# Kernel optimization log

Hardware: AMD Instinct MI355X
Metric: run time of the kernel (lower is better)

## Reference

```python
import jax, jax.numpy as jnp
import numpy as np

EPS_NORM = 1e-12  # F.normalize eps

def _weight_norm(v, g):
    # torch weight_norm with dim=0: W[o,:] = g[o] * v[o,:] / ||v[o,:]||
    return g[:, None] * v / jnp.linalg.norm(v, axis=1, keepdims=True)

def _l2_normalize(x, axis):
    n = jnp.linalg.norm(x, axis=axis, keepdims=True)
    return x / jnp.maximum(n, EPS_NORM)

def setup_inputs() -> dict:
    key = jax.random.key(0)
    ks = jax.random.split(key, 6)
    B, C_emb, T = 16, 1024, 2048
    K, C_cb = 4096, 64
    return {
        "x": jax.random.normal(ks[0], (B, C_emb, T), dtype=jnp.float32),
        "v_in": jax.random.normal(ks[1], (C_cb, C_emb), dtype=jnp.float32) * 0.02,
        "g_in": jax.random.uniform(ks[2], (C_cb,), dtype=jnp.float32, minval=0.5, maxval=1.5),
        "v_out": jax.random.normal(ks[3], (C_emb, C_cb), dtype=jnp.float32) * 0.02,
        "g_out": jax.random.uniform(ks[4], (C_emb,), dtype=jnp.float32, minval=0.5, maxval=1.5),
        "codebook": jax.random.normal(ks[5], (K, C_cb), dtype=jnp.float32),
    }

def reference(x, v_in, g_in, v_out, g_out, codebook):
    sg = jax.lax.stop_gradient
    W_in = _weight_norm(v_in, g_in)    # (C_cb, C_emb)
    W_out = _weight_norm(v_out, g_out)  # (C_emb, C_cb)

    # 1x1 conv projection: (B, C_cb, T)
    x_proj = jnp.einsum('oi,bit->bot', W_in, x)

    # normalize=True: cosine-style nearest neighbor
    emb = _l2_normalize(x_proj, axis=1)           # (B, C_cb, T)
    cb_n = _l2_normalize(codebook, axis=1)        # (K, C_cb)

    e = jnp.swapaxes(emb, 1, 2)                   # (B, T, C_cb)
    # squared euclidean distance (monotone with cdist for argmin)
    dot = jnp.einsum('btc,kc->btk', e, cb_n)      # (B, T, K)
    d2 = (jnp.sum(e * e, axis=-1, keepdims=True)
          - 2.0 * dot
          + jnp.sum(cb_n * cb_n, axis=-1))
    codes = jnp.argmin(d2, axis=-1)               # (B, T) int

    # gather from the UN-normalized codebook (matches torch code)
    quantized_e = codebook[codes]                 # (B, T, C_cb)
    q = jnp.swapaxes(quantized_e, 1, 2)           # (B, C_cb, T)

    codebook_loss = jnp.mean((sg(x_proj) - q) ** 2)
    commit_loss = jnp.mean((x_proj - sg(q)) ** 2)

    quantized_proj = x_proj + sg(q - x_proj)      # straight-through
    quantized = jnp.einsum('oc,bct->bot', W_out, quantized_proj)  # (B, C_emb, T)

    return codes, quantized, codebook_loss, commit_loss, x_proj, quantized_proj
```

## Files before the change

kernel.cpp:

```cpp
#include <hip/hip_runtime.h>
#include <math.h>

#define BB 16
#define CE 1024
#define TT 2048
#define KK 4096
#define CC 64

#define O_CODES 0
#define O_QUANT 32768
#define O_CBL   33587200
#define O_CML   33587201
#define O_XPROJ 33587202
#define O_QPROJ 35684354

#define W_WINF  0
#define W_WOUTF 262144
#define W_CBSQ  327680
#define W_LOSS  659456
#define W_BF    659520

typedef __attribute__((ext_vector_type(8))) _Float16 half8;
typedef __attribute__((ext_vector_type(4))) float f32x4;

__global__ __launch_bounds__(64) void prep_kernel(
    const float* __restrict__ v_in, const float* __restrict__ g_in,
    const float* __restrict__ v_out, const float* __restrict__ g_out,
    const float* __restrict__ cb, float* __restrict__ ws) {
  int bid = blockIdx.x, tid = threadIdx.x;
  if (bid == 0 && tid == 0) ws[W_LOSS] = 0.f;
  if (bid < 64) {
    int o = bid;
    float s = 0.f;
    for (int i = tid; i < CE; i += 64) { float v = v_in[o * CE + i]; s += v * v; }
    for (int off = 32; off; off >>= 1) s += __shfl_down(s, off);
    s = __shfl(s, 0);
    float norm = sqrtf(s);
    float g = g_in[o];
    _Float16* wf = (_Float16*)(ws + W_WINF);
    int ot = o >> 4, m = o & 15;
    for (int i = tid; i < CE; i += 64) {
      float w = (g * v_in[o * CE + i]) / norm;
      _Float16 hi = (_Float16)w;
      _Float16 lo = (_Float16)(w - (float)hi);
      int ks = i >> 5, q = (i >> 3) & 3, j = i & 7;
      int lane = q * 16 + m;
      int base = ((ot * 32 + ks) * 64 + lane) * 8 + j;
      wf[base] = hi;
      wf[65536 + base] = lo;
    }
  } else if (bid < 64 + CE) {
    int o = bid - 64;
    int c = tid;
    float v = v_out[o * CC + c];
    float s = v * v;
    for (int off = 32; off; off >>= 1) s += __shfl_down(s, off);
    s = __shfl(s, 0);
    float w = (g_out[o] * v) / sqrtf(s);
    _Float16 hi = (_Float16)w;
    _Float16 lo = (_Float16)(w - (float)hi);
    _Float16* wf = (_Float16*)(ws + W_WOUTF);
    int ot = o >> 4, m = o & 15;
    int ks = c >> 5, q = (c >> 3) & 3, j = c & 7;
    int lane = q * 16 + m;
    int base = ((ot * 2 + ks) * 64 + lane) * 8 + j;
    wf[base] = hi;
    wf[131072 / 2 + base] = lo;
  } else {
    int k = bid - 64 - CE;
    int c = tid;
    float v = cb[k * CC + c];
    float s = v * v;
    for (int off = 32; off; off >>= 1) s += __shfl_down(s, off);
    s = __shfl(s, 0);
    float n = fmaxf(sqrtf(s), 1e-12f);
    float cn = v / n;
    float s2 = cn * cn;
    for (int off = 32; off; off >>= 1) s2 += __shfl_down(s2, off);
    if (tid == 0) ws[W_CBSQ + k] = s2;
    _Float16 hi = (_Float16)cn;
    _Float16 lo = (_Float16)(cn - (float)hi);
    _Float16* bfh = (_Float16*)(ws + W_BF);
    int ntile = k >> 4, ki = c >> 5;
    int lane = ((c >> 3) & 3) * 16 + (k & 15);
    int j = c & 7;
    int idx = (((ntile * 2 + ki) * 64 + lane) << 3) + j;
    bfh[idx] = hi;
    bfh[262144 + idx] = lo;
  }
}

__global__ __launch_bounds__(512, 2) void fused_kernel(
    const float* __restrict__ x, const float* __restrict__ cb,
    const float* __restrict__ ws, float* __restrict__ out,
    float* loss_acc) {
  __shared__ float xls[64][68];
  __shared__ float nrmS[64];
  __shared__ float pbS[8][64];
  __shared__ int   piS[8][64];
  __shared__ int   codeS[64];

  int tid = threadIdx.x;
  int w = tid >> 6, l = tid & 63;
  int n = l & 15, q = l >> 4;
  int blk = blockIdx.x;
  int b = blk >> 5, t0 = (blk & 31) * 64;

  const half8* wfin = (const half8*)(ws + W_WINF);
  const half8* wfo  = (const half8*)(ws + W_WOUTF);
  const half8* bfr  = (const half8*)(ws + W_BF);
  const float* cbsq = ws + W_CBSQ;

  if (w < 4) {
    int t = t0 + w * 16 + n;
    const float* xp = x + (size_t)b * CE * TT + t;
    f32x4 acc[4];
#pragma unroll
    for (int ot = 0; ot < 4; ++ot) acc[ot] = (f32x4){0.f, 0.f, 0.f, 0.f};

    float v[2][8];
    half8 wh[2][4], wl[2][4];
#pragma unroll
    for (int j = 0; j < 8; ++j) v[0][j] = xp[(size_t)(q * 8 + j) * TT];
#pragma unroll
    for (int ot = 0; ot < 4; ++ot) {
      wh[0][ot] = wfin[(ot * 32 + 0) * 64 + l];
      wl[0][ot] = wfin[8192 + (ot * 32 + 0) * 64 + l];
    }
#pragma unroll 2
    for (int ks = 0; ks < 32; ++ks) {
      int cur = ks & 1;
      if (ks < 31) {
        int kb = (ks + 1) * 32 + q * 8;
#pragma unroll
        for (int j = 0; j < 8; ++j) v[cur ^ 1][j] = xp[(size_t)(kb + j) * TT];
#pragma unroll
        for (int ot = 0; ot < 4; ++ot) {
          wh[cur ^ 1][ot] = wfin[(ot * 32 + ks + 1) * 64 + l];
          wl[cur ^ 1][ot] = wfin[8192 + (ot * 32 + ks + 1) * 64 + l];
        }
      }
      half8 xh, xl;
#pragma unroll
      for (int j = 0; j < 8; ++j) xh[j] = (_Float16)v[cur][j];
#pragma unroll
      for (int j = 0; j < 8; ++j) xl[j] = (_Float16)(v[cur][j] - (float)xh[j]);
#pragma unroll
      for (int ot = 0; ot < 4; ++ot)
        acc[ot] = __builtin_amdgcn_mfma_f32_16x16x32_f16(wh[cur][ot], xh, acc[ot], 0, 0, 0);
#pragma unroll
      for (int ot = 0; ot < 4; ++ot)
        acc[ot] = __builtin_amdgcn_mfma_f32_16x16x32_f16(wh[cur][ot], xl, acc[ot], 0, 0, 0);
#pragma unroll
      for (int ot = 0; ot < 4; ++ot)
        acc[ot] = __builtin_amdgcn_mfma_f32_16x16x32_f16(wl[cur][ot], xh, acc[ot], 0, 0, 0);
    }

    float s = 0.f;
    int tl = w * 16 + n;
#pragma unroll
    for (int ot = 0; ot < 4; ++ot) {
#pragma unroll
      for (int r = 0; r < 4; ++r) {
        float vv = acc[ot][r];
        out[O_XPROJ + (size_t)(b * CC + ot * 16 + q * 4 + r) * TT + t] = vv;
        s = fmaf(vv, vv, s);
      }
      *(f32x4*)&xls[tl][ot * 16 + q * 4] = acc[ot];
    }
    s += __shfl_xor(s, 16);
    s += __shfl_xor(s, 32);
    if (l < 16) nrmS[tl] = fmaxf(sqrtf(s), 1e-12f);
  }
  __syncthreads();

  {
    half8 Ahi[4][2], Alo[4][2];
#pragma unroll
    for (int bd = 0; bd < 4; ++bd) {
      int tl = bd * 16 + n;
      float nv = nrmS[tl];
#pragma unroll
      for (int ki = 0; ki < 2; ++ki) {
#pragma unroll
        for (int j = 0; j < 8; ++j) {
          float vv = xls[tl][ki * 32 + q * 8 + j] / nv;
          _Float16 h = (_Float16)vv;
          Ahi[bd][ki][j] = h;
          Alo[bd][ki][j] = (_Float16)(vv - (float)h);
        }
      }
    }

    float best[4][4];
    int bidx[4][4];
#pragma unroll
    for (int bd = 0; bd < 4; ++bd)
#pragma unroll
      for (int r = 0; r < 4; ++r) { best[bd][r] = 3.4e38f; bidx[bd][r] = 0; }

    half8 Bh0[2], Bh1[2], Bl0[2], Bl1[2];
    float cq[2];
    int ntb = w * 32;
    {
      int nt = ntb;
      Bh0[0] = bfr[(nt * 2 + 0) * 64 + l];
      Bh1[0] = bfr[(nt * 2 + 1) * 64 + l];
      Bl0[0] = bfr[32768 + (nt * 2 + 0) * 64 + l];
      Bl1[0] = bfr[32768 + (nt * 2 + 1) * 64 + l];
      cq[0] = cbsq[nt * 16 + n];
    }
#pragma unroll 2
    for (int it = 0; it < 32; ++it) {
      int cur = it & 1;
      int nt = ntb + it;
      if (it < 31) {
        int nt2 = nt + 1;
        Bh0[cur ^ 1] = bfr[(nt2 * 2 + 0) * 64 + l];
        Bh1[cur ^ 1] = bfr[(nt2 * 2 + 1) * 64 + l];
        Bl0[cur ^ 1] = bfr[32768 + (nt2 * 2 + 0) * 64 + l];
        Bl1[cur ^ 1] = bfr[32768 + (nt2 * 2 + 1) * 64 + l];
        cq[cur ^ 1] = cbsq[nt2 * 16 + n];
      }
      f32x4 acc[4];
#pragma unroll
      for (int bd = 0; bd < 4; ++bd) acc[bd] = (f32x4){0.f, 0.f, 0.f, 0.f};
#pragma unroll
      for (int bd = 0; bd < 4; ++bd)
        acc[bd] = __builtin_amdgcn_mfma_f32_16x16x32_f16(Ahi[bd][0], Bh0[cur], acc[bd], 0, 0, 0);
#pragma unroll
      for (int bd = 0; bd < 4; ++bd)
        acc[bd] = __builtin_amdgcn_mfma_f32_16x16x32_f16(Ahi[bd][1], Bh1[cur], acc[bd], 0, 0, 0);
#pragma unroll
      for (int bd = 0; bd < 4; ++bd)
        acc[bd] = __builtin_amdgcn_mfma_f32_16x16x32_f16(Alo[bd][0], Bh0[cur], acc[bd], 0, 0, 0);
#pragma unroll
      for (int bd = 0; bd < 4; ++bd)
        acc[bd] = __builtin_amdgcn_mfma_f32_16x16x32_f16(Alo[bd][1], Bh1[cur], acc[bd], 0, 0, 0);
#pragma unroll
      for (int bd = 0; bd < 4; ++bd)
        acc[bd] = __builtin_amdgcn_mfma_f32_16x16x32_f16(Ahi[bd][0], Bl0[cur], acc[bd], 0, 0, 0);
#pragma unroll
      for (int bd = 0; bd < 4; ++bd)
        acc[bd] = __builtin_amdgcn_mfma_f32_16x16x32_f16(Ahi[bd][1], Bl1[cur], acc[bd], 0, 0, 0);

      int kl = nt * 16 + n;
#pragma unroll
      for (int bd = 0; bd < 4; ++bd)
#pragma unroll
        for (int r = 0; r < 4; ++r) {
          float sc = fmaf(-2.f, acc[bd][r], cq[cur]);
          if (sc < best[bd][r]) { best[bd][r] = sc; bidx[bd][r] = kl; }
        }
    }

#pragma unroll
    for (int st = 1; st < 16; st <<= 1) {
#pragma unroll
      for (int bd = 0; bd < 4; ++bd)
#pragma unroll
        for (int r = 0; r < 4; ++r) {
          float os = __shfl_xor(best[bd][r], st);
          int oi = __shfl_xor(bidx[bd][r], st);
          if (os < best[bd][r] || (os == best[bd][r] && oi < bidx[bd][r])) {
            best[bd][r] = os;
            bidx[bd][r] = oi;
          }
        }
    }
    if (n == 0) {
#pragma unroll
      for (int bd = 0; bd < 4; ++bd)
#pragma unroll
        for (int r = 0; r < 4; ++r) {
          int tl = bd * 16 + q * 4 + r;
          pbS[w][tl] = best[bd][r];
          piS[w][tl] = bidx[bd][r];
        }
    }
  }
  __syncthreads();

  if (tid < 64) {
    float bs = pbS[0][tid];
    int bi = piS[0][tid];
#pragma unroll
    for (int s = 1; s < 8; ++s) {
      float s2 = pbS[s][tid];
      int i2 = piS[s][tid];
      if (s2 < bs || (s2 == bs && i2 < bi)) { bs = s2; bi = i2; }
    }
    codeS[tid] = bi;
    out[O_CODES + b * TT + t0 + tid] = (float)bi;
  }
  __syncthreads();

  {
    int tg = w & 3, oh = w >> 2;
    int t = t0 + tg * 16 + n;
    int tl = tg * 16 + n;
    int code = codeS[tl];
    const float* cbr = cb + (size_t)code * CC;
    float qv[2][8];
#pragma unroll
    for (int ks = 0; ks < 2; ++ks) {
      float4 a = *(const float4*)&cbr[ks * 32 + q * 8];
      float4 c4 = *(const float4*)&cbr[ks * 32 + q * 8 + 4];
      qv[ks][0] = a.x; qv[ks][1] = a.y; qv[ks][2] = a.z; qv[ks][3] = a.w;
      qv[ks][4] = c4.x; qv[ks][5] = c4.y; qv[ks][6] = c4.z; qv[ks][7] = c4.w;
    }

    if (oh == 0) {
      float ls = 0.f;
#pragma unroll
      for (int ks = 0; ks < 2; ++ks)
#pragma unroll
        for (int j = 0; j < 8; ++j) {
          int c = ks * 32 + q * 8 + j;
          float qq = qv[ks][j];
          out[O_QPROJ + (size_t)(b * CC + c) * TT + t] = qq;
          float d = xls[tl][c] - qq;
          ls = fmaf(d, d, ls);
        }
      for (int off = 32; off; off >>= 1) ls += __shfl_down(ls, off);
      if (l == 0) atomicAdd(loss_acc, ls);
    }

    half8 qh[2], ql[2];
#pragma unroll
    for (int ks = 0; ks < 2; ++ks)
#pragma unroll
      for (int j = 0; j < 8; ++j) {
        qh[ks][j] = (_Float16)qv[ks][j];
        ql[ks][j] = (_Float16)(qv[ks][j] - (float)qh[ks][j]);
      }

    int ob = oh * 32;
    half8 wc[2][4];
    wc[0][0] = wfo[(ob * 2 + 0) * 64 + l];
    wc[0][1] = wfo[(ob * 2 + 1) * 64 + l];
    wc[0][2] = wfo[8192 + (ob * 2 + 0) * 64 + l];
    wc[0][3] = wfo[8192 + (ob * 2 + 1) * 64 + l];
#pragma unroll 2
    for (int i = 0; i < 32; ++i) {
      int cur = i & 1;
      int ot = ob + i;
      if (i < 31) {
        int o2 = ot + 1;
        wc[cur ^ 1][0] = wfo[(o2 * 2 + 0) * 64 + l];
        wc[cur ^ 1][1] = wfo[(o2 * 2 + 1) * 64 + l];
        wc[cur ^ 1][2] = wfo[8192 + (o2 * 2 + 0) * 64 + l];
        wc[cur ^ 1][3] = wfo[8192 + (o2 * 2 + 1) * 64 + l];
      }
      f32x4 acc = (f32x4){0.f, 0.f, 0.f, 0.f};
      acc = __builtin_amdgcn_mfma_f32_16x16x32_f16(wc[cur][0], qh[0], acc, 0, 0, 0);
      acc = __builtin_amdgcn_mfma_f32_16x16x32_f16(wc[cur][1], qh[1], acc, 0, 0, 0);
      acc = __builtin_amdgcn_mfma_f32_16x16x32_f16(wc[cur][0], ql[0], acc, 0, 0, 0);
      acc = __builtin_amdgcn_mfma_f32_16x16x32_f16(wc[cur][1], ql[1], acc, 0, 0, 0);
      acc = __builtin_amdgcn_mfma_f32_16x16x32_f16(wc[cur][2], qh[0], acc, 0, 0, 0);
      acc = __builtin_amdgcn_mfma_f32_16x16x32_f16(wc[cur][3], qh[1], acc, 0, 0, 0);
#pragma unroll
      for (int r = 0; r < 4; ++r)
        out[O_QUANT + (size_t)(b * CE + ot * 16 + q * 4 + r) * TT + t] = acc[r];
    }
  }
}

__global__ void finalize_kernel(const float* __restrict__ ws, float* __restrict__ out) {
  if (threadIdx.x == 0 && blockIdx.x == 0) {
    float l = ws[W_LOSS] / 2097152.f;
    out[O_CBL] = l;
    out[O_CML] = l;
  }
}

extern "C" void kernel_launch(void* const* d_in, const int* in_sizes, int n_in,
                              void* d_out, int out_size, void* d_ws, size_t ws_size,
                              hipStream_t stream) {
  const float* x     = (const float*)d_in[0];
  const float* v_in  = (const float*)d_in[1];
  const float* g_in  = (const float*)d_in[2];
  const float* v_out = (const float*)d_in[3];
  const float* g_out = (const float*)d_in[4];
  const float* cb    = (const float*)d_in[5];
  float* out = (float*)d_out;
  float* ws  = (float*)d_ws;

  prep_kernel<<<64 + 1024 + 4096, 64, 0, stream>>>(v_in, g_in, v_out, g_out, cb, ws);
  fused_kernel<<<512, 512, 0, stream>>>(x, cb, ws, out, ws + W_LOSS);
  finalize_kernel<<<1, 64, 0, stream>>>(ws, out);
}
```

Baseline: 366.1 us.

## Halve per-block time tile to 32 and split projection across all waves

Blocks now cover 32 timesteps with 256 threads, and the grid grows to 1024 blocks. In the projection phase all four waves take part, each computing half of the output channels for a 16-timestep slice, with the partial squared norms combined through shared memory. Previously only half the waves did this work. Each wave now scans 64 codebook tiles against 2 row blocks instead of 32 tiles against 4. The aim is better CU fill and no idle waves during projection, at the cost of reloading codebook fragments twice as often per timestep and an extra barrier.

```diff
diff --git a/kernel.cpp b/kernel.cpp
--- a/kernel.cpp
+++ b/kernel.cpp
@@ -90,42 +90,45 @@
   }
 }
 
-__global__ __launch_bounds__(512, 2) void fused_kernel(
+__global__ __launch_bounds__(256, 3) void fused_kernel(
     const float* __restrict__ x, const float* __restrict__ cb,
     const float* __restrict__ ws, float* __restrict__ out,
     float* loss_acc) {
-  __shared__ float xls[64][68];
-  __shared__ float nrmS[64];
-  __shared__ float pbS[8][64];
-  __shared__ int   piS[8][64];
-  __shared__ int   codeS[64];
+  __shared__ float xls[32][68];
+  __shared__ float nrmP[2][2][16];
+  __shared__ float nrmS[32];
+  __shared__ float pbS[4][32];
+  __shared__ int   piS[4][32];
+  __shared__ int   codeS[32];
 
   int tid = threadIdx.x;
   int w = tid >> 6, l = tid & 63;
   int n = l & 15, q = l >> 4;
   int blk = blockIdx.x;
-  int b = blk >> 5, t0 = (blk & 31) * 64;
+  int b = blk >> 6, t0 = (blk & 63) * 32;
 
   const half8* wfin = (const half8*)(ws + W_WINF);
   const half8* wfo  = (const half8*)(ws + W_WOUTF);
   const half8* bfr  = (const half8*)(ws + W_BF);
   const float* cbsq = ws + W_CBSQ;
 
-  if (w < 4) {
-    int t = t0 + w * 16 + n;
+  {
+    int tt = w & 1, oh = w >> 1;
+    int t = t0 + tt * 16 + n;
+    int tl = tt * 16 + n;
     const float* xp = x + (size_t)b * CE * TT + t;
-    f32x4 acc[4];
-#pragma unroll
-    for (int ot = 0; ot < 4; ++ot) acc[ot] = (f32x4){0.f, 0.f, 0.f, 0.f};
+    f32x4 acc[2];
+#pragma unroll
+    for (int ot2 = 0; ot2 < 2; ++ot2) acc[ot2] = (f32x4){0.f, 0.f, 0.f, 0.f};
 
     float v[2][8];
-    half8 wh[2][4], wl[2][4];
+    half8 wh[2][2], wl[2][2];
 #pragma unroll
     for (int j = 0; j < 8; ++j) v[0][j] = xp[(size_t)(q * 8 + j) * TT];
 #pragma unroll
-    for (int ot = 0; ot < 4; ++ot) {
-      wh[0][ot] = wfin[(ot * 32 + 0) * 64 + l];
-      wl[0][ot] = wfin[8192 + (ot * 32 + 0) * 64 + l];
+    for (int ot2 = 0; ot2 < 2; ++ot2) {
+      wh[0][ot2] = wfin[((oh * 2 + ot2) * 32 + 0) * 64 + l];
+      wl[0][ot2] = wfin[8192 + ((oh * 2 + ot2) * 32 + 0) * 64 + l];
     }
 #pragma unroll 2
     for (int ks = 0; ks < 32; ++ks) {
@@ -135,9 +138,9 @@
 #pragma unroll
         for (int j = 0; j < 8; ++j) v[cur ^ 1][j] = xp[(size_t)(kb + j) * TT];
 #pragma unroll
-        for (int ot = 0; ot < 4; ++ot) {
-          wh[cur ^ 1][ot] = wfin[(ot * 32 + ks + 1) * 64 + l];
-          wl[cur ^ 1][ot] = wfin[8192 + (ot * 32 + ks + 1) * 64 + l];
+        for (int ot2 = 0; ot2 < 2; ++ot2) {
+          wh[cur ^ 1][ot2] = wfin[((oh * 2 + ot2) * 32 + ks + 1) * 64 + l];
+          wl[cur ^ 1][ot2] = wfin[8192 + ((oh * 2 + ot2) * 32 + ks + 1) * 64 + l];
         }
       }
       half8 xh, xl;
@@ -146,38 +149,41 @@
 #pragma unroll
       for (int j = 0; j < 8; ++j) xl[j] = (_Float16)(v[cur][j] - (float)xh[j]);
 #pragma unroll
-      for (int ot = 0; ot < 4; ++ot)
-        acc[ot] = __builtin_amdgcn_mfma_f32_16x16x32_f16(wh[cur][ot], xh, acc[ot], 0, 0, 0);
-#pragma unroll
-      for (int ot = 0; ot < 4; ++ot)
-        acc[ot] = __builtin_amdgcn_mfma_f32_16x16x32_f16(wh[cur][ot], xl, acc[ot], 0, 0, 0);
-#pragma unroll
-      for (int ot = 0; ot < 4; ++ot)
-        acc[ot] = __builtin_amdgcn_mfma_f32_16x16x32_f16(wl[cur][ot], xh, acc[ot], 0, 0, 0);
+      for (int ot2 = 0; ot2 < 2; ++ot2)
+        acc[ot2] = __builtin_amdgcn_mfma_f32_16x16x32_f16(wh[cur][ot2], xh, acc[ot2], 0, 0, 0);
+#pragma unroll
+      for (int ot2 = 0; ot2 < 2; ++ot2)
+        acc[ot2] = __builtin_amdgcn_mfma_f32_16x16x32_f16(wh[cur][ot2], xl, acc[ot2], 0, 0, 0);
+#pragma unroll
+      for (int ot2 = 0; ot2 < 2; ++ot2)
+        acc[ot2] = __builtin_amdgcn_mfma_f32_16x16x32_f16(wl[cur][ot2], xh, acc[ot2], 0, 0, 0);
     }
 
     float s = 0.f;
-    int tl = w * 16 + n;
-#pragma unroll
-    for (int ot = 0; ot < 4; ++ot) {
+#pragma unroll
+    for (int ot2 = 0; ot2 < 2; ++ot2) {
+      int oc = (oh * 2 + ot2) * 16 + q * 4;
 #pragma unroll
       for (int r = 0; r < 4; ++r) {
-        float vv = acc[ot][r];
-        out[O_XPROJ + (size_t)(b * CC + ot * 16 + q * 4 + r) * TT + t] = vv;
+        float vv = acc[ot2][r];
+        out[O_XPROJ + (size_t)(b * CC + oc + r) * TT + t] = vv;
         s = fmaf(vv, vv, s);
       }
-      *(f32x4*)&xls[tl][ot * 16 + q * 4] = acc[ot];
+      *(f32x4*)&xls[tl][oc] = acc[ot2];
     }
     s += __shfl_xor(s, 16);
     s += __shfl_xor(s, 32);
-    if (l < 16) nrmS[tl] = fmaxf(sqrtf(s), 1e-12f);
+    if (l < 16) nrmP[tt][oh][l] = s;
   }
   __syncthreads();
+  if (tid < 32)
+    nrmS[tid] = fmaxf(sqrtf(nrmP[tid >> 4][0][tid & 15] + nrmP[tid >> 4][1][tid & 15]), 1e-12f);
+  __syncthreads();
 
   {
-    half8 Ahi[4][2], Alo[4][2];
-#pragma unroll
-    for (int bd = 0; bd < 4; ++bd) {
+    half8 Ahi[2][2], Alo[2][2];
+#pragma unroll
+    for (int bd = 0; bd < 2; ++bd) {
       int tl = bd * 16 + n;
       float nv = nrmS[tl];
 #pragma unroll
@@ -192,16 +198,16 @@
       }
     }
 
-    float best[4][4];
-    int bidx[4][4];
-#pragma unroll
-    for (int bd = 0; bd < 4; ++bd)
+    float best[2][4];
+    int bidx[2][4];
+#pragma unroll
+    for (int bd = 0; bd < 2; ++bd)
 #pragma unroll
       for (int r = 0; r < 4; ++r) { best[bd][r] = 3.4e38f; bidx[bd][r] = 0; }
 
     half8 Bh0[2], Bh1[2], Bl0[2], Bl1[2];
     float cq[2];
-    int ntb = w * 32;
+    int ntb = w * 64;
     {
       int nt = ntb;
       Bh0[0] = bfr[(nt * 2 + 0) * 64 + l];
@@ -211,10 +217,10 @@
       cq[0] = cbsq[nt * 16 + n];
     }
 #pragma unroll 2
-    for (int it = 0; it < 32; ++it) {
+    for (int it = 0; it < 64; ++it) {
       int cur = it & 1;
       int nt = ntb + it;
-      if (it < 31) {
+      if (it < 63) {
         int nt2 = nt + 1;
         Bh0[cur ^ 1] = bfr[(nt2 * 2 + 0) * 64 + l];
         Bh1[cur ^ 1] = bfr[(nt2 * 2 + 1) * 64 + l];
@@ -222,31 +228,31 @@
         Bl1[cur ^ 1] = bfr[32768 + (nt2 * 2 + 1) * 64 + l];
         cq[cur ^ 1] = cbsq[nt2 * 16 + n];
       }
-      f32x4 acc[4];
-#pragma unroll
-      for (int bd = 0; bd < 4; ++bd) acc[bd] = (f32x4){0.f, 0.f, 0.f, 0.f};
-#pragma unroll
-      for (int bd = 0; bd < 4; ++bd)
+      f32x4 acc[2];
+#pragma unroll
+      for (int bd = 0; bd < 2; ++bd) acc[bd] = (f32x4){0.f, 0.f, 0.f, 0.f};
+#pragma unroll
+      for (int bd = 0; bd < 2; ++bd)
         acc[bd] = __builtin_amdgcn_mfma_f32_16x16x32_f16(Ahi[bd][0], Bh0[cur], acc[bd], 0, 0, 0);
 #pragma unroll
-      for (int bd = 0; bd < 4; ++bd)
+      for (int bd = 0; bd < 2; ++bd)
         acc[bd] = __builtin_amdgcn_mfma_f32_16x16x32_f16(Ahi[bd][1], Bh1[cur], acc[bd], 0, 0, 0);
 #pragma unroll
-      for (int bd = 0; bd < 4; ++bd)
+      for (int bd = 0; bd < 2; ++bd)
         acc[bd] = __builtin_amdgcn_mfma_f32_16x16x32_f16(Alo[bd][0], Bh0[cur], acc[bd], 0, 0, 0);
 #pragma unroll
-      for (int bd = 0; bd < 4; ++bd)
+      for (int bd = 0; bd < 2; ++bd)
         acc[bd] = __builtin_amdgcn_mfma_f32_16x16x32_f16(Alo[bd][1], Bh1[cur], acc[bd], 0, 0, 0);
 #pragma unroll
-      for (int bd = 0; bd < 4; ++bd)
+      for (int bd = 0; bd < 2; ++bd)
         acc[bd] = __builtin_amdgcn_mfma_f32_16x16x32_f16(Ahi[bd][0], Bl0[cur], acc[bd], 0, 0, 0);
 #pragma unroll
-      for (int bd = 0; bd < 4; ++bd)
+      for (int bd = 0; bd < 2; ++bd)
         acc[bd] = __builtin_amdgcn_mfma_f32_16x16x32_f16(Ahi[bd][1], Bl1[cur], acc[bd], 0, 0, 0);
 
       int kl = nt * 16 + n;
 #pragma unroll
-      for (int bd = 0; bd < 4; ++bd)
+      for (int bd = 0; bd < 2; ++bd)
 #pragma unroll
         for (int r = 0; r < 4; ++r) {
           float sc = fmaf(-2.f, acc[bd][r], cq[cur]);
@@ -257,7 +263,7 @@
 #pragma unroll
     for (int st = 1; st < 16; st <<= 1) {
 #pragma unroll
-      for (int bd = 0; bd < 4; ++bd)
+      for (int bd = 0; bd < 2; ++bd)
 #pragma unroll
         for (int r = 0; r < 4; ++r) {
           float os = __shfl_xor(best[bd][r], st);
@@ -270,7 +276,7 @@
     }
     if (n == 0) {
 #pragma unroll
-      for (int bd = 0; bd < 4; ++bd)
+      for (int bd = 0; bd < 2; ++bd)
 #pragma unroll
         for (int r = 0; r < 4; ++r) {
           int tl = bd * 16 + q * 4 + r;
@@ -281,11 +287,11 @@
   }
   __syncthreads();
 
-  if (tid < 64) {
+  if (tid < 32) {
     float bs = pbS[0][tid];
     int bi = piS[0][tid];
 #pragma unroll
-    for (int s = 1; s < 8; ++s) {
+    for (int s = 1; s < 4; ++s) {
       float s2 = pbS[s][tid];
       int i2 = piS[s][tid];
       if (s2 < bs || (s2 == bs && i2 < bi)) { bs = s2; bi = i2; }
@@ -296,9 +302,9 @@
   __syncthreads();
 
   {
-    int tg = w & 3, oh = w >> 2;
-    int t = t0 + tg * 16 + n;
-    int tl = tg * 16 + n;
+    int tt = w & 1, oh = w >> 1;
+    int t = t0 + tt * 16 + n;
+    int tl = tt * 16 + n;
     int code = codeS[tl];
     const float* cbr = cb + (size_t)code * CC;
     float qv[2][8];
@@ -387,6 +393,6 @@
   float* ws  = (float*)d_ws;
 
   prep_kernel<<<64 + 1024 + 4096, 64, 0, stream>>>(v_in, g_in, v_out, g_out, cb, ws);
-  fused_kernel<<<512, 512, 0, stream>>>(x, cb, ws, out, ws + W_LOSS);
+  fused_kernel<<<1024, 256, 0, stream>>>(x, cb, ws, out, ws + W_LOSS);
   finalize_kernel<<<1, 64, 0, stream>>>(ws, out);
 }
```

Result: no change. 370.0 us (+1.0%).
